# Kernel optimization log

Hardware: AMD Instinct MI355X
Metric: run time of the kernel (lower is better)

The kernel has to match this reference:

```python
import jax, jax.numpy as jnp
import numpy as np

K = 3
PAD = 1
KK = K * K
GROUPS = 32  # min(32, dim) with dim=64
EPS = 1e-5


def _conv(x, w, pad):
    return jax.lax.conv_general_dilated(
        x, w, (1, 1), [(pad, pad), (pad, pad)],
        dimension_numbers=('NCHW', 'OIHW', 'NCHW'))


def _bilinear_gather(x, py, px):
    # x: (B,C,H,W); py,px: (B,KK,H,W) float sampling coords (zero pad outside)
    B, C, H, W = x.shape
    xf = x.reshape(B, C, H * W)
    y0f = jnp.floor(py)
    x0f = jnp.floor(px)
    wy1 = py - y0f  # fractional weights (differentiable path to offsets)
    wx1 = px - x0f
    y0 = y0f.astype(jnp.int32)
    x0 = x0f.astype(jnp.int32)

    def g(yi, xi):
        valid = (yi >= 0) & (yi < H) & (xi >= 0) & (xi < W)
        idx = (jnp.clip(yi, 0, H - 1) * W + jnp.clip(xi, 0, W - 1)).reshape(B, 1, -1)
        v = jnp.take_along_axis(xf, idx, axis=2).reshape(B, C, KK, H, W)
        return v * valid[:, None].astype(x.dtype)

    v00 = g(y0, x0)
    v01 = g(y0, x0 + 1)
    v10 = g(y0 + 1, x0)
    v11 = g(y0 + 1, x0 + 1)
    wy1e = wy1[:, None]
    wx1e = wx1[:, None]
    return (v00 * (1 - wy1e) * (1 - wx1e) + v01 * (1 - wy1e) * wx1e
            + v10 * wy1e * (1 - wx1e) + v11 * wy1e * wx1e)


def _forward(x, w_off1, w_off2, w_mask1, w_mask2, weight, bias, gamma, beta):
    B, C, H, W = x.shape
    # offset branch: 1x1 conv then KxK conv -> (B, 2*KK, H, W)
    off = _conv(_conv(x, w_off1, 0), w_off2, PAD).reshape(B, KK, 2, H, W)
    # mask branch -> sigmoid modulation (B, KK, H, W)
    mask = jax.nn.sigmoid(_conv(_conv(x, w_mask1, 0), w_mask2, PAD))
    # base kernel grid (torchvision deform_conv2d: pairs are (dy, dx) per tap)
    ky = jnp.repeat(jnp.arange(K) - PAD, K).astype(x.dtype)
    kx = jnp.tile(jnp.arange(K) - PAD, K).astype(x.dtype)
    py = off[:, :, 0] + jnp.arange(H, dtype=x.dtype)[None, None, :, None] + ky[None, :, None, None]
    px = off[:, :, 1] + jnp.arange(W, dtype=x.dtype)[None, None, None, :] + kx[None, :, None, None]
    samp = _bilinear_gather(x, py, px)  # (B, C, KK, H, W)
    # depthwise deformable conv: per-channel weight over KK taps, modulated by mask
    out = jnp.einsum('bkhw,ck,bckhw->bchw', mask, weight.reshape(C, KK), samp)
    out = out + bias[None, :, None, None]
    # GroupNorm(32, C)
    g = out.reshape(B, GROUPS, C // GROUPS, H, W)
    mu = g.mean(axis=(2, 3, 4), keepdims=True)
    var = g.var(axis=(2, 3, 4), keepdims=True)
    gn = ((g - mu) * jax.lax.rsqrt(var + EPS)).reshape(B, C, H, W)
    gn = gn * gamma[None, :, None, None] + beta[None, :, None, None]
    return jax.nn.gelu(gn, approximate=False)


def setup_inputs() -> dict:
    key = jax.random.key(0)
    ks = jax.random.split(key, 6)
    B, C, H, W = 4, 64, 128, 128
    x = jax.random.normal(ks[0], (B, C, H, W), dtype=jnp.float32)
    w_off1 = jax.random.normal(ks[1], (C, C, 1, 1), dtype=jnp.float32) * 0.05
    w_off2 = jax.random.normal(ks[2], (2 * KK, C, K, K), dtype=jnp.float32) * 0.02
    w_mask1 = jax.random.normal(ks[3], (C, C, 1, 1), dtype=jnp.float32) * 0.05
    w_mask2 = jax.random.normal(ks[4], (KK, C, K, K), dtype=jnp.float32) * 0.05
    bound = 1.0 / np.sqrt(KK)  # kaiming_uniform(a=1) for (C,1,K,K) -> fan_in=KK
    weight = jax.random.uniform(ks[5], (C, 1, K, K), dtype=jnp.float32,
                                minval=-bound, maxval=bound)
    bias = jnp.zeros((C,), dtype=jnp.float32)
    gamma = jnp.ones((C,), dtype=jnp.float32)
    beta = jnp.zeros((C,), dtype=jnp.float32)
    return {'x': x, 'w_off1': w_off1, 'w_off2': w_off2, 'w_mask1': w_mask1,
            'w_mask2': w_mask2, 'weight': weight, 'bias': bias,
            'gamma': gamma, 'beta': beta}


def reference(x, w_off1, w_off2, w_mask1, w_mask2, weight, bias, gamma, beta):
    return _forward(x, w_off1, w_off2, w_mask1, w_mask2, weight, bias, gamma, beta)
```

## Files before the change

### kernel.cpp

```cpp
#include <hip/hip_runtime.h>
#include <math.h>

#define B_  4
#define C_  64
#define H_  128
#define W_  128
#define HW_ (H_*W_)
#define NPIX_ (B_*HW_)
#define GROUPS_ 32

typedef __attribute__((ext_vector_type(8))) short short8;
typedef __attribute__((ext_vector_type(4))) float f32x4;

__device__ inline short f2bf_rne(float f) {
    unsigned u = __float_as_uint(f);
    unsigned r = (u + 0x7FFFu + ((u >> 16) & 1u)) >> 16;
    return (short)r;
}
__device__ inline short8 ld8(const short* p) {
    union { uint4 u; short8 s; } c;
    c.u = *(const uint4*)p;
    return c.s;
}

__global__ __launch_bounds__(256) void k01(const float* __restrict__ x,
                                           const float* __restrict__ w_off1,
                                           const float* __restrict__ w_mask1,
                                           const float* __restrict__ w_off2,
                                           const float* __restrict__ w_mask2,
                                           short* __restrict__ xtb,
                                           short* __restrict__ wc_hi) {
    if (blockIdx.x >= 1024) {
        int i = (blockIdx.x - 1024) * 256 + threadIdx.x;
        if (i < 32 * 576) {
            int cout = i / 576;
            int r    = i % 576;
            int pos  = r >> 6, ci = r & 63;
            float s = 0.f;
            if (cout < 18) {
                for (int cm = 0; cm < 64; cm++)
                    s += w_off2[(cout * 64 + cm) * 9 + pos] * w_off1[cm * 64 + ci];
            } else if (cout < 27) {
                for (int cm = 0; cm < 64; cm++)
                    s += w_mask2[((cout - 18) * 64 + cm) * 9 + pos] * w_mask1[cm * 64 + ci];
            }
            wc_hi[i] = f2bf_rne(s);
        }
        return;
    }
    int l   = threadIdx.x & 63;
    int wv  = threadIdx.x >> 6;
    int row = l >> 4, col = l & 15;
    int p0  = blockIdx.x * 64 + wv * 16;
    int b   = p0 >> 14;
    int hw  = p0 & (HW_ - 1);
    const float* xb = x + (size_t)b * C_ * HW_ + hw;
#pragma unroll
    for (int kb = 0; kb < 2; kb++) {
        int ci0 = kb * 32 + row * 8;
        float xv[8];
#pragma unroll
        for (int j = 0; j < 8; j++) xv[j] = xb[(ci0 + j) * HW_ + col];
        short8 a;
#pragma unroll
        for (int j = 0; j < 8; j++) a[j] = f2bf_rne(xv[j]);
        union { short8 s; uint4 u; } cv; cv.s = a;
        *(uint4*)(xtb + ((size_t)(p0 + col)) * 64 + ci0) = cv.u;
    }
}

__global__ __launch_bounds__(256, 2) void k2_mfma(const short* __restrict__ xtb,
                                                  const short* __restrict__ wc_hi,
                                                  float* __restrict__ offmask) {
    int l   = threadIdx.x & 63;
    int wv  = threadIdx.x >> 6;
    int row = l >> 4, col = l & 15;
    int blk = blockIdx.x;
    int h   = blk & 127;
    int pb  = blk * 128 + wv * 32;
    int w0  = (pb & 127);

    short8 wfr[18][2];
#pragma unroll
    for (int kb = 0; kb < 18; kb++) {
        int pos = kb >> 1;
        int ci0 = (kb & 1) * 32 + row * 8;
        int ko  = pos * 64 + ci0;
        wfr[kb][0] = ld8(wc_hi + (size_t)col * 576 + ko);
        wfr[kb][1] = ld8(wc_hi + (size_t)(col + 16) * 576 + ko);
    }

    const short8 zero = {0,0,0,0,0,0,0,0};
    f32x4 a00 = {0.f,0.f,0.f,0.f};
    f32x4 a01 = {0.f,0.f,0.f,0.f};
    f32x4 a10 = {0.f,0.f,0.f,0.f};
    f32x4 a11 = {0.f,0.f,0.f,0.f};

    short8 ca0, ca1;
    {
        const int dy = -1, dx = -1;
        int ci0 = row * 8;
#pragma unroll
        for (int mt = 0; mt < 2; mt++) {
            int pbase = pb + mt * 16 + col;
            int w = w0 + mt * 16 + col;
            bool valid = ((unsigned)(h + dy) < 128u) && ((unsigned)(w + dx) < 128u);
            int addr = valid ? (pbase + dy * 128 + dx) : pbase;
            short8 v = ld8(xtb + (size_t)addr * 64 + ci0);
            if (mt == 0) ca0 = valid ? v : zero; else ca1 = valid ? v : zero;
        }
    }

#pragma unroll
    for (int kb = 0; kb < 18; kb++) {
        short8 na0, na1;
        if (kb < 17) {
            const int kn = kb + 1;
            const int pos = kn >> 1;
            const int dy = pos / 3 - 1, dx = pos % 3 - 1;
            int ci0 = (kn & 1) * 32 + row * 8;
#pragma unroll
            for (int mt = 0; mt < 2; mt++) {
                int pbase = pb + mt * 16 + col;
                int w = w0 + mt * 16 + col;
                bool valid = ((unsigned)(h + dy) < 128u) && ((unsigned)(w + dx) < 128u);
                int addr = valid ? (pbase + dy * 128 + dx) : pbase;
                short8 v = ld8(xtb + (size_t)addr * 64 + ci0);
                if (mt == 0) na0 = valid ? v : zero; else na1 = valid ? v : zero;
            }
        }
        a00 = __builtin_amdgcn_mfma_f32_16x16x32_bf16(ca0, wfr[kb][0], a00, 0, 0, 0);
        a01 = __builtin_amdgcn_mfma_f32_16x16x32_bf16(ca0, wfr[kb][1], a01, 0, 0, 0);
        a10 = __builtin_amdgcn_mfma_f32_16x16x32_bf16(ca1, wfr[kb][0], a10, 0, 0, 0);
        a11 = __builtin_amdgcn_mfma_f32_16x16x32_bf16(ca1, wfr[kb][1], a11, 0, 0, 0);
        ca0 = na0; ca1 = na1;
    }

#pragma unroll
    for (int mt = 0; mt < 2; mt++) {
        f32x4 n0 = mt ? a10 : a00;
        f32x4 n1 = mt ? a11 : a01;
#pragma unroll
        for (int r = 0; r < 4; r++) {
            int p = pb + mt * 16 + row * 4 + r;
            float* om = offmask + (size_t)p * 32;
            om[col] = n0[r];
            if (col < 2)       om[16 + col] = n1[r];
            else if (col < 11) om[16 + col] = 1.f / (1.f + expf(-n1[r]));
        }
    }
}

__global__ __launch_bounds__(256) void k3_deform(const short* __restrict__ xtb,
                                                 const float* __restrict__ offmask,
                                                 const float* __restrict__ weight,
                                                 const float* __restrict__ bias,
                                                 unsigned short* __restrict__ out_pre,
                                                 float* __restrict__ partials) {
    __shared__ float wl[C_ * 9];
    __shared__ float bl[C_];
    __shared__ float lds_s[4][4][8];
    __shared__ float lds_ss[4][4][8];
    for (int i = threadIdx.x; i < C_ * 9; i += 256) wl[i] = weight[i];
    if (threadIdx.x < C_) bl[threadIdx.x] = bias[threadIdx.x];
    __syncthreads();

    int blk   = blockIdx.x;
    int xcd   = blk & 7;
    int slot  = blk >> 3;
    int b     = slot >> 5;
    int r     = (slot & 31) >> 1;
    int hrow  = slot & 1;
    int h     = xcd * 16 + r;
    int pl    = threadIdx.x >> 2;
    int chunk = threadIdx.x & 3;
    int c0    = chunk * 16;
    int w     = hrow * 64 + pl;
    int hw    = h * W_ + w;
    int P     = b * HW_ + hw;
    int slot_img = xcd * 32 + (slot & 31);

    float acc[16];
#pragma unroll
    for (int i = 0; i < 16; i++) acc[i] = 0.f;

    const float* po = offmask + (size_t)P * 32;
    const short* xb = xtb + (size_t)b * HW_ * 64;

    for (int k = 0; k < 9; k++) {
        float offy = po[2 * k];
        float offx = po[2 * k + 1];
        float mk   = po[18 + k];
        float py = offy + (float)h + (float)(k / 3 - 1);
        float px = offx + (float)w + (float)(k % 3 - 1);
        float y0f = floorf(py), x0f = floorf(px);
        int y0 = (int)y0f, x0 = (int)x0f;
        int y1 = y0 + 1,   x1 = x0 + 1;
        float wy1 = py - y0f, wx1 = px - x0f;
        float wy0 = 1.f - wy1, wx0 = 1.f - wx1;
        bool vy0 = ((unsigned)y0 < (unsigned)H_);
        bool vy1 = ((unsigned)y1 < (unsigned)H_);
        bool vx0 = ((unsigned)x0 < (unsigned)W_);
        bool vx1 = ((unsigned)x1 < (unsigned)W_);
        int cy0 = min(max(y0, 0), H_ - 1);
        int cy1 = min(max(y1, 0), H_ - 1);
        int cx0 = min(max(x0, 0), W_ - 1);
        int cx1 = min(max(x1, 0), W_ - 1);
        float b00 = wy0 * wx0 * ((vy0 && vx0) ? mk : 0.f);
        float b01 = wy0 * wx1 * ((vy0 && vx1) ? mk : 0.f);
        float b10 = wy1 * wx0 * ((vy1 && vx0) ? mk : 0.f);
        float b11 = wy1 * wx1 * ((vy1 && vx1) ? mk : 0.f);

        const short* p00 = xb + ((size_t)cy0 * W_ + cx0) * 64 + c0;
        const short* p01 = xb + ((size_t)cy0 * W_ + cx1) * 64 + c0;
        const short* p10 = xb + ((size_t)cy1 * W_ + cx0) * 64 + c0;
        const short* p11 = xb + ((size_t)cy1 * W_ + cx1) * 64 + c0;

#pragma unroll
        for (int half = 0; half < 2; half++) {
            uint4 u00 = *(const uint4*)(p00 + 8 * half);
            uint4 u01 = *(const uint4*)(p01 + 8 * half);
            uint4 u10 = *(const uint4*)(p10 + 8 * half);
            uint4 u11 = *(const uint4*)(p11 + 8 * half);
            unsigned a00[4] = {u00.x, u00.y, u00.z, u00.w};
            unsigned a01[4] = {u01.x, u01.y, u01.z, u01.w};
            unsigned a10[4] = {u10.x, u10.y, u10.z, u10.w};
            unsigned a11[4] = {u11.x, u11.y, u11.z, u11.w};
#pragma unroll
            for (int d = 0; d < 4; d++) {
                float s_lo = b00 * __uint_as_float(a00[d] << 16)
                           + b01 * __uint_as_float(a01[d] << 16)
                           + b10 * __uint_as_float(a10[d] << 16)
                           + b11 * __uint_as_float(a11[d] << 16);
                float s_hi = b00 * __uint_as_float(a00[d] & 0xFFFF0000u)
                           + b01 * __uint_as_float(a01[d] & 0xFFFF0000u)
                           + b10 * __uint_as_float(a10[d] & 0xFFFF0000u)
                           + b11 * __uint_as_float(a11[d] & 0xFFFF0000u);
                int c = 8 * half + 2 * d;
                acc[c]     += wl[(c0 + c) * 9 + k] * s_lo;
                acc[c + 1] += wl[(c0 + c + 1) * 9 + k] * s_hi;
            }
        }
    }

    unsigned short* op = out_pre + ((size_t)b * C_ + c0) * HW_ + hw;
#pragma unroll
    for (int c = 0; c < 16; c++) {
        acc[c] += bl[c0 + c];
        op[c * HW_] = (unsigned short)f2bf_rne(acc[c]);
    }

    float s8[8], ss8[8];
#pragma unroll
    for (int j = 0; j < 8; j++) {
        float a0 = acc[2 * j], a1 = acc[2 * j + 1];
        s8[j]  = a0 + a1;
        ss8[j] = a0 * a0 + a1 * a1;
    }
#pragma unroll
    for (int m = 4; m < 64; m <<= 1) {
#pragma unroll
        for (int j = 0; j < 8; j++) {
            s8[j]  += __shfl_xor(s8[j], m);
            ss8[j] += __shfl_xor(ss8[j], m);
        }
    }
    int lane = threadIdx.x & 63, wid = threadIdx.x >> 6;
    if (lane < 4) {
#pragma unroll
        for (int j = 0; j < 8; j++) {
            lds_s[wid][lane][j]  = s8[j];
            lds_ss[wid][lane][j] = ss8[j];
        }
    }
    __syncthreads();
    if (threadIdx.x < 32) {
        int g = threadIdx.x;
        int ch = g >> 3, j = g & 7;
        float S  = lds_s[0][ch][j] + lds_s[1][ch][j] + lds_s[2][ch][j] + lds_s[3][ch][j];
        float SS = lds_ss[0][ch][j] + lds_ss[1][ch][j] + lds_ss[2][ch][j] + lds_ss[3][ch][j];
        float2 v = make_float2(S, SS);
        *(float2*)(partials + (((size_t)(b * GROUPS_ + g)) * 256 + slot_img) * 2) = v;
    }
}

__global__ __launch_bounds__(256) void k4_reduce(const float* __restrict__ partials,
                                                 float* __restrict__ stats) {
    int bg = blockIdx.x;
    float2 v = ((const float2*)partials)[bg * 256 + threadIdx.x];
    float s = v.x, ss = v.y;
#pragma unroll
    for (int m = 1; m < 64; m <<= 1) {
        s  += __shfl_xor(s, m);
        ss += __shfl_xor(ss, m);
    }
    __shared__ float ls[8];
    int lane = threadIdx.x & 63, wid = threadIdx.x >> 6;
    if (lane == 0) { ls[wid] = s; ls[4 + wid] = ss; }
    __syncthreads();
    if (threadIdx.x == 0) {
        float S  = ls[0] + ls[1] + ls[2] + ls[3];
        float SS = ls[4] + ls[5] + ls[6] + ls[7];
        const float inv = 1.f / (2.f * HW_);
        float mean = S * inv;
        float var  = SS * inv - mean * mean;
        stats[bg * 2]     = mean;
        stats[bg * 2 + 1] = rsqrtf(var + 1e-5f);
    }
}

__global__ __launch_bounds__(256) void k5_norm_gelu(const unsigned short* __restrict__ out_pre,
                                                    const float* __restrict__ stats,
                                                    const float* __restrict__ gamma,
                                                    const float* __restrict__ beta,
                                                    float* __restrict__ out) {
    int i = blockIdx.x * 256 + threadIdx.x;
    int e = i << 3;
    int c = (e >> 14) & (C_ - 1);
    int b = e >> 20;
    int bg = b * GROUPS_ + (c >> 1);
    float mean = stats[bg * 2];
    float rstd = stats[bg * 2 + 1];
    float ga = gamma[c] * rstd;
    float be = beta[c] - mean * ga;
    uint4 v = ((const uint4*)out_pre)[i];
    unsigned dw[4] = {v.x, v.y, v.z, v.w};
    float o[8];
#pragma unroll
    for (int d = 0; d < 4; d++) {
        float lo = __uint_as_float(dw[d] << 16);
        float hi = __uint_as_float(dw[d] & 0xFFFF0000u);
        float t0 = lo * ga + be;
        float t1 = hi * ga + be;
        o[2 * d]     = 0.5f * t0 * (1.f + erff(t0 * 0.70710678118654752f));
        o[2 * d + 1] = 0.5f * t1 * (1.f + erff(t1 * 0.70710678118654752f));
    }
    ((float4*)out)[2 * i]     = make_float4(o[0], o[1], o[2], o[3]);
    ((float4*)out)[2 * i + 1] = make_float4(o[4], o[5], o[6], o[7]);
}

extern "C" void kernel_launch(void* const* d_in, const int* in_sizes, int n_in,
                              void* d_out, int out_size, void* d_ws, size_t ws_size,
                              hipStream_t stream) {
    const float* x       = (const float*)d_in[0];
    const float* w_off1  = (const float*)d_in[1];
    const float* w_off2  = (const float*)d_in[2];
    const float* w_mask1 = (const float*)d_in[3];
    const float* w_mask2 = (const float*)d_in[4];
    const float* weight  = (const float*)d_in[5];
    const float* bias    = (const float*)d_in[6];
    const float* gamma   = (const float*)d_in[7];
    const float* beta    = (const float*)d_in[8];
    float* out = (float*)d_out;

    char* ws = (char*)d_ws;
    size_t o = 0;
    short* wc_hi = (short*)(ws + o); o += 32 * 576 * 2;
    o = (o + 255) & ~(size_t)255;
    short* xtb               = (short*)(ws + o);          o += (size_t)NPIX_ * 64 * 2;
    float* offmask           = (float*)(ws + o);          o += (size_t)NPIX_ * 32 * 4;
    unsigned short* out_pre  = (unsigned short*)(ws + o); o += (size_t)NPIX_ * 64 * 2;
    float* partials          = (float*)(ws + o);          o += (size_t)128 * 256 * 2 * 4;
    float* stats             = (float*)(ws + o);          o += 256 * 4;

    hipLaunchKernelGGL(k01, dim3(1024 + 72), dim3(256), 0, stream,
                       x, w_off1, w_mask1, w_off2, w_mask2, xtb, wc_hi);
    hipLaunchKernelGGL(k2_mfma, dim3(NPIX_ / 128), dim3(256), 0, stream,
                       xtb, wc_hi, offmask);
    hipLaunchKernelGGL(k3_deform, dim3(NPIX_ / 64), dim3(256), 0, stream,
                       xtb, offmask, weight, bias, out_pre, partials);
    hipLaunchKernelGGL(k4_reduce, dim3(B_ * GROUPS_), dim3(256), 0, stream,
                       partials, stats);
    hipLaunchKernelGGL(k5_norm_gelu, dim3(NPIX_ * 64 / 8 / 256), dim3(256), 0, stream,
                       out_pre, stats, gamma, beta, out);
}
```

Before: 136.0 us.

## Stage 16x16 halo tile in LDS for deform gather; fold group stats via atomics

The deform kernel now handles 8x8 pixel tiles and first copies a 16x16 pixel neighborhood (all 64 bf16 channels, padded stride) into shared memory. Bilinear taps read from LDS when they land inside it and fall back to global memory otherwise. This is meant to cut scattered global gathers. The separate partial-sum reduction kernel is also removed: blocks atomically add group sums into a buffer zeroed in k01, and the norm kernel computes mean and rstd itself. The costs are larger LDS use, a divergent fallback path, and atomic contention plus nondeterministic summation order.

```diff
diff --git a/kernel.cpp b/kernel.cpp
--- a/kernel.cpp
+++ b/kernel.cpp
@@ -29,8 +29,10 @@
                                            const float* __restrict__ w_off2,
                                            const float* __restrict__ w_mask2,
                                            short* __restrict__ xtb,
-                                           short* __restrict__ wc_hi) {
+                                           short* __restrict__ wc_hi,
+                                           float* __restrict__ stats_raw) {
     if (blockIdx.x >= 1024) {
+        if (blockIdx.x == 1024) stats_raw[threadIdx.x] = 0.f;
         int i = (blockIdx.x - 1024) * 256 + threadIdx.x;
         if (i < 32 * 576) {
             int cout = i / 576;
@@ -151,41 +153,54 @@
     }
 }
 
-__global__ __launch_bounds__(256) void k3_deform(const short* __restrict__ xtb,
-                                                 const float* __restrict__ offmask,
-                                                 const float* __restrict__ weight,
-                                                 const float* __restrict__ bias,
-                                                 unsigned short* __restrict__ out_pre,
-                                                 float* __restrict__ partials) {
+__global__ __launch_bounds__(256, 4) void k3_deform(const short* __restrict__ xtb,
+                                                    const float* __restrict__ offmask,
+                                                    const float* __restrict__ weight,
+                                                    const float* __restrict__ bias,
+                                                    unsigned short* __restrict__ out_pre,
+                                                    float* __restrict__ stats_raw) {
+    __shared__ unsigned short sx[16 * 16 * 72];
     __shared__ float wl[C_ * 9];
     __shared__ float bl[C_];
     __shared__ float lds_s[4][4][8];
     __shared__ float lds_ss[4][4][8];
+
+    int blk  = blockIdx.x;
+    int b    = blk >> 8;
+    int tile = blk & 255;
+    int h0   = (tile >> 4) * 8;
+    int w0   = (tile & 15) * 8;
+
+    const short* xb = xtb + (size_t)b * HW_ * 64;
+
     for (int i = threadIdx.x; i < C_ * 9; i += 256) wl[i] = weight[i];
     if (threadIdx.x < C_) bl[threadIdx.x] = bias[threadIdx.x];
+
+    {
+        int t  = threadIdx.x;
+        int gy = min(max(h0 - 4 + (t >> 4), 0), H_ - 1);
+        int gx = min(max(w0 - 4 + (t & 15), 0), W_ - 1);
+        const short* gp = xb + ((size_t)gy * W_ + gx) * 64;
+        unsigned short* sp = &sx[t * 72];
+#pragma unroll
+        for (int j = 0; j < 8; j++)
+            *(uint4*)(sp + j * 8) = *(const uint4*)(gp + j * 8);
+    }
     __syncthreads();
 
-    int blk   = blockIdx.x;
-    int xcd   = blk & 7;
-    int slot  = blk >> 3;
-    int b     = slot >> 5;
-    int r     = (slot & 31) >> 1;
-    int hrow  = slot & 1;
-    int h     = xcd * 16 + r;
     int pl    = threadIdx.x >> 2;
     int chunk = threadIdx.x & 3;
     int c0    = chunk * 16;
-    int w     = hrow * 64 + pl;
+    int h     = h0 + (pl >> 3);
+    int w     = w0 + (pl & 7);
     int hw    = h * W_ + w;
     int P     = b * HW_ + hw;
-    int slot_img = xcd * 32 + (slot & 31);
 
     float acc[16];
 #pragma unroll
     for (int i = 0; i < 16; i++) acc[i] = 0.f;
 
     const float* po = offmask + (size_t)P * 32;
-    const short* xb = xtb + (size_t)b * HW_ * 64;
 
     for (int k = 0; k < 9; k++) {
         float offy = po[2 * k];
@@ -211,21 +226,29 @@
         float b10 = wy1 * wx0 * ((vy1 && vx0) ? mk : 0.f);
         float b11 = wy1 * wx1 * ((vy1 && vx1) ? mk : 0.f);
 
-        const short* p00 = xb + ((size_t)cy0 * W_ + cx0) * 64 + c0;
-        const short* p01 = xb + ((size_t)cy0 * W_ + cx1) * 64 + c0;
-        const short* p10 = xb + ((size_t)cy1 * W_ + cx0) * 64 + c0;
-        const short* p11 = xb + ((size_t)cy1 * W_ + cx1) * 64 + c0;
+        uint4 u[4][2];
+        int cys[4] = {cy0, cy0, cy1, cy1};
+        int cxs[4] = {cx0, cx1, cx0, cx1};
+#pragma unroll
+        for (int cn = 0; cn < 4; cn++) {
+            int ry = cys[cn] - (h0 - 4), rx = cxs[cn] - (w0 - 4);
+            if (((unsigned)ry < 16u) && ((unsigned)rx < 16u)) {
+                const unsigned short* p = &sx[(ry * 16 + rx) * 72 + c0];
+                u[cn][0] = *(const uint4*)(p);
+                u[cn][1] = *(const uint4*)(p + 8);
+            } else {
+                const short* p = xb + ((size_t)cys[cn] * W_ + cxs[cn]) * 64 + c0;
+                u[cn][0] = *(const uint4*)(p);
+                u[cn][1] = *(const uint4*)(p + 8);
+            }
+        }
 
 #pragma unroll
         for (int half = 0; half < 2; half++) {
-            uint4 u00 = *(const uint4*)(p00 + 8 * half);
-            uint4 u01 = *(const uint4*)(p01 + 8 * half);
-            uint4 u10 = *(const uint4*)(p10 + 8 * half);
-            uint4 u11 = *(const uint4*)(p11 + 8 * half);
-            unsigned a00[4] = {u00.x, u00.y, u00.z, u00.w};
-            unsigned a01[4] = {u01.x, u01.y, u01.z, u01.w};
-            unsigned a10[4] = {u10.x, u10.y, u10.z, u10.w};
-            unsigned a11[4] = {u11.x, u11.y, u11.z, u11.w};
+            unsigned a00[4] = {u[0][half].x, u[0][half].y, u[0][half].z, u[0][half].w};
+            unsigned a01[4] = {u[1][half].x, u[1][half].y, u[1][half].z, u[1][half].w};
+            unsigned a10[4] = {u[2][half].x, u[2][half].y, u[2][half].z, u[2][half].w};
+            unsigned a11[4] = {u[3][half].x, u[3][half].y, u[3][half].z, u[3][half].w};
 #pragma unroll
             for (int d = 0; d < 4; d++) {
                 float s_lo = b00 * __uint_as_float(a00[d] << 16)
@@ -279,38 +302,13 @@
         int ch = g >> 3, j = g & 7;
         float S  = lds_s[0][ch][j] + lds_s[1][ch][j] + lds_s[2][ch][j] + lds_s[3][ch][j];
         float SS = lds_ss[0][ch][j] + lds_ss[1][ch][j] + lds_ss[2][ch][j] + lds_ss[3][ch][j];
-        float2 v = make_float2(S, SS);
-        *(float2*)(partials + (((size_t)(b * GROUPS_ + g)) * 256 + slot_img) * 2) = v;
-    }
-}
-
-__global__ __launch_bounds__(256) void k4_reduce(const float* __restrict__ partials,
-                                                 float* __restrict__ stats) {
-    int bg = blockIdx.x;
-    float2 v = ((const float2*)partials)[bg * 256 + threadIdx.x];
-    float s = v.x, ss = v.y;
-#pragma unroll
-    for (int m = 1; m < 64; m <<= 1) {
-        s  += __shfl_xor(s, m);
-        ss += __shfl_xor(ss, m);
-    }
-    __shared__ float ls[8];
-    int lane = threadIdx.x & 63, wid = threadIdx.x >> 6;
-    if (lane == 0) { ls[wid] = s; ls[4 + wid] = ss; }
-    __syncthreads();
-    if (threadIdx.x == 0) {
-        float S  = ls[0] + ls[1] + ls[2] + ls[3];
-        float SS = ls[4] + ls[5] + ls[6] + ls[7];
-        const float inv = 1.f / (2.f * HW_);
-        float mean = S * inv;
-        float var  = SS * inv - mean * mean;
-        stats[bg * 2]     = mean;
-        stats[bg * 2 + 1] = rsqrtf(var + 1e-5f);
+        atomicAdd(&stats_raw[(b * GROUPS_ + g) * 2],     S);
+        atomicAdd(&stats_raw[(b * GROUPS_ + g) * 2 + 1], SS);
     }
 }
 
 __global__ __launch_bounds__(256) void k5_norm_gelu(const unsigned short* __restrict__ out_pre,
-                                                    const float* __restrict__ stats,
+                                                    const float* __restrict__ stats_raw,
                                                     const float* __restrict__ gamma,
                                                     const float* __restrict__ beta,
                                                     float* __restrict__ out) {
@@ -319,8 +317,12 @@
     int c = (e >> 14) & (C_ - 1);
     int b = e >> 20;
     int bg = b * GROUPS_ + (c >> 1);
-    float mean = stats[bg * 2];
-    float rstd = stats[bg * 2 + 1];
+    float S  = stats_raw[bg * 2];
+    float SS = stats_raw[bg * 2 + 1];
+    const float inv = 1.f / (2.f * HW_);
+    float mean = S * inv;
+    float var  = SS * inv - mean * mean;
+    float rstd = rsqrtf(var + 1e-5f);
     float ga = gamma[c] * rstd;
     float be = beta[c] - mean * ga;
     uint4 v = ((const uint4*)out_pre)[i];
@@ -360,17 +362,14 @@
     short* xtb               = (short*)(ws + o);          o += (size_t)NPIX_ * 64 * 2;
     float* offmask           = (float*)(ws + o);          o += (size_t)NPIX_ * 32 * 4;
     unsigned short* out_pre  = (unsigned short*)(ws + o); o += (size_t)NPIX_ * 64 * 2;
-    float* partials          = (float*)(ws + o);          o += (size_t)128 * 256 * 2 * 4;
-    float* stats             = (float*)(ws + o);          o += 256 * 4;
+    float* stats_raw         = (float*)(ws + o);          o += 256 * 4;
 
     hipLaunchKernelGGL(k01, dim3(1024 + 72), dim3(256), 0, stream,
-                       x, w_off1, w_mask1, w_off2, w_mask2, xtb, wc_hi);
+                       x, w_off1, w_mask1, w_off2, w_mask2, xtb, wc_hi, stats_raw);
     hipLaunchKernelGGL(k2_mfma, dim3(NPIX_ / 128), dim3(256), 0, stream,
                        xtb, wc_hi, offmask);
-    hipLaunchKernelGGL(k3_deform, dim3(NPIX_ / 64), dim3(256), 0, stream,
-                       xtb, offmask, weight, bias, out_pre, partials);
-    hipLaunchKernelGGL(k4_reduce, dim3(B_ * GROUPS_), dim3(256), 0, stream,
-                       partials, stats);
+    hipLaunchKernelGGL(k3_deform, dim3(1024), dim3(256), 0, stream,
+                       xtb, offmask, weight, bias, out_pre, stats_raw);
     hipLaunchKernelGGL(k5_norm_gelu, dim3(NPIX_ * 64 / 8 / 256), dim3(256), 0, stream,
-                       out_pre, stats, gamma, beta, out);
-}
+                       out_pre, stats_raw, gamma, beta, out);
+}
```

After: 152.6 us. +12.2%, slower.
